# Performance work log

Measured on AMD Instinct MI355X. Metric: run time of the kernel, lower is better.

The kernel has to match this reference:

```python
import jax, jax.numpy as jnp
import numpy as np

E = 768; H = 64; W = 64; K = 3; PAD = 1
CH = [30, 100, 150, 220, 268]


def _conv3x3(x, w, b):
    out = jax.lax.conv_general_dilated(x, w, (1, 1), ((PAD, PAD), (PAD, PAD)),
                                       dimension_numbers=('NCHW', 'OIHW', 'NCHW'))
    return out + b[None, :, None, None]


def _deform_conv(x, offset, mask, w, b):
    # modulated deform_conv2d, group=1, stride=1, dil=1, pad=1 (torchvision semantics)
    N, C, Hh, Ww = x.shape
    KK = K * K
    off = offset.reshape(N, KK, 2, Hh, Ww)  # [...,0]=dy, [...,1]=dx per kernel tap
    ky = jnp.repeat(jnp.arange(K), K).astype(x.dtype)
    kx = jnp.tile(jnp.arange(K), K).astype(x.dtype)
    hg = jnp.arange(Hh, dtype=x.dtype)[None, None, :, None]
    wg = jnp.arange(Ww, dtype=x.dtype)[None, None, None, :]
    py = hg - PAD + ky[None, :, None, None] + off[:, :, 0]  # [N,9,H,W]
    px = wg - PAD + kx[None, :, None, None] + off[:, :, 1]
    y0 = jnp.floor(py); x0 = jnp.floor(px)
    xf = x.reshape(N, C, Hh * Ww)

    def gather(yi, xi):
        valid = ((yi >= 0) & (yi <= Hh - 1) & (xi >= 0) & (xi <= Ww - 1)).astype(x.dtype)
        yc = jnp.clip(yi, 0, Hh - 1).astype(jnp.int32)
        xc = jnp.clip(xi, 0, Ww - 1).astype(jnp.int32)
        idx = (yc * Ww + xc).reshape(N, 1, KK * Hh * Ww)
        g = jnp.take_along_axis(xf, idx, axis=2).reshape(N, C, KK, Hh, Ww)
        return g * valid[:, None]

    wy1 = py - y0; wx1 = px - x0; wy0 = 1.0 - wy1; wx0 = 1.0 - wx1
    samp = (gather(y0, x0) * (wy0 * wx0)[:, None]
            + gather(y0, x0 + 1) * (wy0 * wx1)[:, None]
            + gather(y0 + 1, x0) * (wy1 * wx0)[:, None]
            + gather(y0 + 1, x0 + 1) * (wy1 * wx1)[:, None])
    samp = samp * mask[:, None]  # modulation
    out = jnp.einsum('nckhw,ock->nohw', samp, w.reshape(w.shape[0], C, KK))
    return out + b[None, :, None, None]


def _block(x, conv_w, conv_b, off_w, off_b, msk_w, msk_b, bn_g, bn_b):
    # DefConv2d.forward: conv -> offset/mask linears -> deform conv -> BN(train stats) -> relu
    N, C, Hh, Ww = x.shape
    om = _conv3x3(x, conv_w, conv_b)
    om_hwc = om.transpose(0, 2, 3, 1)
    offset = (om_hwc @ off_w.T + off_b).transpose(0, 3, 1, 2)  # [N,18,H,W]
    mask = jax.nn.softmax(om_hwc @ msk_w.T + msk_b, axis=-1)   # [N,H,W,9]
    mask = mask.reshape(N, K * K, Hh, Ww)  # raw reshape, exactly as torch .reshape (no permute)
    out = _deform_conv(x, offset, mask, conv_w, conv_b)
    mu = out.mean(axis=(0, 2, 3), keepdims=True)
    var = out.var(axis=(0, 2, 3), keepdims=True)
    out = (out - mu) / jnp.sqrt(var + 1e-5) * bn_g[None, :, None, None] + bn_b[None, :, None, None]
    return jax.nn.relu(out)


def _cam(x, chq_w, chv_w, chz_w, ln_g, ln_b, spq_w, spv_w):
    xin = x
    N, C, Hh, Ww = x.shape  # N must be 1 (matches torch reshapes)
    # channel attention
    wv = jnp.einsum('nchw,oc->nohw', x, chv_w).reshape(C // 2, Hh * Ww)
    wq = jax.nn.softmax(jnp.einsum('nchw,oc->nohw', x, chq_w).reshape(Hh * Ww))
    wz = chz_w @ (wv @ wq)  # [C]
    wz = (wz - wz.mean()) / jnp.sqrt(wz.var() + 1e-5) * ln_g + ln_b
    x = jax.nn.sigmoid(wz)[None, :, None, None] * x
    # spatial attention
    wq = jax.nn.softmax(jnp.einsum('nchw,oc->nohw', x, spq_w).max(axis=(2, 3)).reshape(C // 2))
    wv = jnp.einsum('nchw,oc->nohw', x, spv_w).reshape(C // 2, Hh * Ww)
    wz = jax.nn.sigmoid(wq @ wv).reshape(1, 1, Hh, Ww)
    return wz * x + xin


def _forward(x1, x2, x3, x4, x5, conv_w, conv_b, off_w, off_b, msk_w, msk_b, bn_g, bn_b,
             chq_w, chv_w, chz_w, ln_g, ln_b, spq_w, spv_w,
             w1, w2, w3a, w3b, w4a, w4b, w5a, w5b, norm_g, norm_b):
    xper = [t.transpose(0, 3, 1, 2) for t in (x1, x2, x3, x4, x5)]
    blk = lambda t: _block(t, conv_w, conv_b, off_w, off_b, msk_w, msk_b, bn_g, bn_b)
    c1 = lambda t, w: jnp.einsum('nchw,oc->nohw', t, w)
    o1 = c1(blk(xper[0]), w1)
    o2 = c1(blk(xper[1]), w2)
    o3 = c1(blk(xper[2]), w3a) + c1(xper[2], w3b)
    o4 = c1(blk(xper[3]), w4a) + c1(xper[3], w4b)
    o5 = c1(blk(xper[4]), w5a) + c1(xper[4], w5b)
    out = jnp.concatenate((o1, o2, o3, o4, o5), axis=1)  # sum(CH)=768 channels
    out = _cam(out, chq_w, chv_w, chz_w, ln_g, ln_b, spq_w, spv_w)
    out = (out + xper[4]).transpose(0, 2, 3, 1)
    mu = out.mean(-1, keepdims=True)
    var = out.var(-1, keepdims=True)
    return (out - mu) / jnp.sqrt(var + 1e-5) * norm_g + norm_b


def setup_inputs() -> dict:
    key = jax.random.key(0)
    ks = iter(jax.random.split(key, 40))
    rnd = lambda shape, s=0.05: jax.random.normal(next(ks), shape, dtype=jnp.float32) * s
    d = {}
    for i in range(5):
        d[f'x{i+1}'] = jax.random.normal(next(ks), (1, H, W, E), dtype=jnp.float32)
    d['conv_w'] = rnd((E, E, 3, 3), 0.02)
    d['conv_b'] = jnp.zeros((E,), jnp.float32)
    d['off_w'] = rnd((2 * 9, E), 0.01); d['off_b'] = jnp.zeros((18,), jnp.float32)
    d['msk_w'] = rnd((9, E), 0.01); d['msk_b'] = jnp.zeros((9,), jnp.float32)
    d['bn_g'] = jnp.ones((E,), jnp.float32); d['bn_b'] = jnp.zeros((E,), jnp.float32)
    C = sum(CH)  # 768
    d['chq_w'] = rnd((1, C)); d['chv_w'] = rnd((C // 2, C)); d['chz_w'] = rnd((C, C // 2))
    d['ln_g'] = jnp.ones((C,), jnp.float32); d['ln_b'] = jnp.zeros((C,), jnp.float32)
    d['spq_w'] = rnd((C // 2, C)); d['spv_w'] = rnd((C // 2, C))
    d['w1'] = rnd((CH[0], E)); d['w2'] = rnd((CH[1], E))
    d['w3a'] = rnd((CH[2], E)); d['w3b'] = rnd((CH[2], E))
    d['w4a'] = rnd((CH[3], E)); d['w4b'] = rnd((CH[3], E))
    d['w5a'] = rnd((CH[4], E)); d['w5b'] = rnd((CH[4], E))
    d['norm_g'] = jnp.ones((E,), jnp.float32); d['norm_b'] = jnp.zeros((E,), jnp.float32)
    return d


def reference(x1, x2, x3, x4, x5, conv_w, conv_b, off_w, off_b, msk_w, msk_b, bn_g, bn_b,
              chq_w, chv_w, chz_w, ln_g, ln_b, spq_w, spv_w,
              w1, w2, w3a, w3b, w4a, w4b, w5a, w5b, norm_g, norm_b):
    return _forward(x1, x2, x3, x4, x5, conv_w, conv_b, off_w, off_b, msk_w, msk_b, bn_g, bn_b,
                    chq_w, chv_w, chz_w, ln_g, ln_b, spq_w, spv_w,
                    w1, w2, w3a, w3b, w4a, w4b, w5a, w5b, norm_g, norm_b)
```

## Files before the change

kernel.cpp:

```cpp
#include <hip/hip_runtime.h>
#include <cstdint>
#include <cstddef>

#define HW 4096
#define CDIM 768
#define PPIX 4356

typedef unsigned short u16;
typedef __attribute__((ext_vector_type(8))) short short8;
typedef __attribute__((ext_vector_type(4))) float f32x4;

__device__ __forceinline__ float bf2f(u16 u) { return __uint_as_float(((unsigned)u) << 16); }
__device__ __forceinline__ u16 f2bf(float f) {
    unsigned u = __float_as_uint(f);
    unsigned r = (u + 0x7fffu + ((u >> 16) & 1u)) >> 16;
    return (u16)r;
}
__device__ __forceinline__ float lof(unsigned u) { return __uint_as_float(u << 16); }
__device__ __forceinline__ float hif(unsigned u) { return __uint_as_float(u & 0xffff0000u); }
__device__ __forceinline__ int swz(int r) { return ((r >> 1) ^ (r >> 3)) & 3; }

__device__ __forceinline__ void gl16(const u16* g, u16* l) {
    __builtin_amdgcn_global_load_lds(
        (const __attribute__((address_space(1))) unsigned int*)g,
        (__attribute__((address_space(3))) unsigned int*)l, 16, 0, 0);
}

enum GMode { G_CONV = 0, G_PROJ = 2, G_SPAT = 3 };

struct ProjP {
    const u16* b1[5];
    const u16* b2[5];
    int ch[5];
    int choff[5];
};

template <int MODE>
__launch_bounds__(256, 4)
__global__ void k_gemm128(const u16* __restrict__ xpad, const u16* __restrict__ blkA,
                          const u16* __restrict__ Wt, const float* __restrict__ bias,
                          u16* __restrict__ outb, float* __restrict__ outf, ProjP pp) {
    const int z = blockIdx.z;
    const int m0 = blockIdx.x * 128;
    const int n0 = blockIdx.y * 128;

    int Nrows, ntap, choff = 0, ldo = CDIM;
    const u16 *Az = nullptr, *Ac = nullptr, *B1 = nullptr, *B2 = nullptr;
    if constexpr (MODE == G_CONV) {
        Az = xpad + (size_t)z * PPIX * CDIM; B1 = Wt; Nrows = 768; ntap = 9;
    } else if constexpr (MODE == G_PROJ) {
        Ac = blkA + (size_t)z * HW * CDIM;
        Az = xpad + (size_t)z * PPIX * CDIM;
        B1 = pp.b1[z]; B2 = pp.b2[z];
        Nrows = pp.ch[z]; choff = pp.choff[z];
        ntap = B2 ? 2 : 1;
        if (n0 >= Nrows) return;
    } else {
        Ac = blkA; B1 = Wt; Nrows = 384; ntap = 1; ldo = 384;
    }

    __shared__ __align__(16) u16 As[128 * 32];
    __shared__ __align__(16) u16 Bs[128 * 32];

    const int t = threadIdx.x;
    const int lane = t & 63;
    const int wid = t >> 6;
    const int wrow = (wid >> 1) * 64, wcol = (wid & 1) * 64;
    const int lm = lane & 15;
    const int quad = lane >> 4;

    const int rS = t >> 2;
    const int cs0 = (t & 3) ^ swz(rS);
    const int cs1 = (t & 3) ^ swz(64 + rS);

    const u16 *a0 = nullptr, *a1 = nullptr, *a0x = nullptr, *a1x = nullptr;
    if constexpr (MODE == G_CONV) {
        int p0 = m0 + rS, p1 = m0 + 64 + rS;
        a0 = Az + (size_t)(((p0 >> 6)) * 66 + (p0 & 63)) * CDIM + cs0 * 8;
        a1 = Az + (size_t)(((p1 >> 6)) * 66 + (p1 & 63)) * CDIM + cs1 * 8;
    } else if constexpr (MODE == G_PROJ) {
        int p0 = m0 + rS, p1 = m0 + 64 + rS;
        a0 = Ac + (size_t)p0 * CDIM + cs0 * 8;
        a1 = Ac + (size_t)p1 * CDIM + cs1 * 8;
        a0x = Az + (size_t)(((p0 >> 6) + 1) * 66 + (p0 & 63) + 1) * CDIM + cs0 * 8;
        a1x = Az + (size_t)(((p1 >> 6) + 1) * 66 + (p1 & 63) + 1) * CDIM + cs1 * 8;
    } else {
        a0 = Ac + (size_t)(m0 + rS) * CDIM + cs0 * 8;
        a1 = Ac + (size_t)(m0 + 64 + rS) * CDIM + cs1 * 8;
    }
    const u16* b0 = B1 + (size_t)(n0 + rS) * CDIM + cs0 * 8;
    const u16* b1p = B1 + (size_t)(n0 + 64 + rS) * CDIM + cs1 * 8;
    const u16 *c0 = nullptr, *c1 = nullptr;
    if constexpr (MODE == G_PROJ) {
        if (B2) {
            c0 = B2 + (size_t)(n0 + rS) * CDIM + cs0 * 8;
            c1 = B2 + (size_t)(n0 + 64 + rS) * CDIM + cs1 * 8;
        }
    }

    u16* dA0 = &As[(0 * 4 + wid) * 512];
    u16* dA1 = &As[(1 * 4 + wid) * 512];
    u16* dB0 = &Bs[(0 * 4 + wid) * 512];
    u16* dB1 = &Bs[(1 * 4 + wid) * 512];

    f32x4 acc[4][4];
#pragma unroll
    for (int i = 0; i < 4; i++)
#pragma unroll
        for (int j = 0; j < 4; j++) acc[i][j] = (f32x4){0.f, 0.f, 0.f, 0.f};

    const int totS = ntap * 24;
    int tap = 0;
    int tA = 0, tB = 0, kO = 0;

    for (int s = 0; s < totS; ++s) {
        __syncthreads();
        if constexpr (MODE == G_CONV) {
            gl16(a0 + tA + kO, dA0);
            gl16(a1 + tA + kO, dA1);
            gl16(b0 + tB + kO, dB0);
            gl16(b1p + tB + kO, dB1);
        } else if constexpr (MODE == G_PROJ) {
            if (tap == 0) {
                gl16(a0 + kO, dA0);
                gl16(a1 + kO, dA1);
                gl16(b0 + kO, dB0);
                gl16(b1p + kO, dB1);
            } else {
                gl16(a0x + kO, dA0);
                gl16(a1x + kO, dA1);
                gl16(c0 + kO, dB0);
                gl16(c1 + kO, dB1);
            }
        } else {
            gl16(a0 + kO, dA0);
            gl16(a1 + kO, dA1);
            gl16(b0 + kO, dB0);
            gl16(b1p + kO, dB1);
        }
        __syncthreads();
        short8 af[4], bf[4];
#pragma unroll
        for (int i = 0; i < 4; i++) {
            int rr = wrow + i * 16 + lm;
            af[i] = *(const short8*)&As[rr * 32 + ((quad ^ swz(rr)) * 8)];
        }
#pragma unroll
        for (int j = 0; j < 4; j++) {
            int rr = wcol + j * 16 + lm;
            bf[j] = *(const short8*)&Bs[rr * 32 + ((quad ^ swz(rr)) * 8)];
        }
#pragma unroll
        for (int i = 0; i < 4; i++)
#pragma unroll
            for (int j = 0; j < 4; j++)
                acc[i][j] = __builtin_amdgcn_mfma_f32_16x16x32_bf16(af[i], bf[j], acc[i][j], 0, 0, 0);
        tap++;
        if constexpr (MODE == G_CONV) {
            tA += (tap == 3 || tap == 6) ? 64 * CDIM : CDIM;
            tB += CDIM * CDIM;
            if (tap == 9) { tap = 0; tA = 0; tB = 0; kO += 32; }
        } else {
            if (tap == ntap) { tap = 0; kO += 32; }
        }
    }

    if constexpr (MODE == G_CONV) {
        u16* outz = outb + (size_t)z * HW * CDIM;
#pragma unroll
        for (int j = 0; j < 4; j++) {
            int gc = n0 + wcol + j * 16 + lm;
            float bv = bias[gc];
#pragma unroll
            for (int i = 0; i < 4; i++)
#pragma unroll
                for (int r = 0; r < 4; r++) {
                    int gr = m0 + wrow + i * 16 + quad * 4 + r;
                    outz[(size_t)gr * CDIM + gc] = f2bf(acc[i][j][r] + bv);
                }
        }
    } else {
#pragma unroll
        for (int j = 0; j < 4; j++) {
            int gc = n0 + wcol + j * 16 + lm;
            if (gc < Nrows) {
#pragma unroll
                for (int i = 0; i < 4; i++)
#pragma unroll
                    for (int r = 0; r < 4; r++) {
                        int gr = m0 + wrow + i * 16 + quad * 4 + r;
                        outf[(size_t)gr * ldo + choff + gc] = acc[i][j][r];
                    }
            }
        }
    }
}

__device__ __forceinline__ void xcd_decode(int bid, int& m0, int& n0, int& z) {
    int work = (bid & 7) * 60 + (bid >> 3);
    z = work / 96;
    int rem = work - z * 96;
    n0 = (rem >> 5) * 256;
    m0 = (rem & 31) * 128;
}

__global__ void k_fold(const u16* __restrict__ Wt, const float* __restrict__ off_w,
                       const float* __restrict__ msk_w, u16* __restrict__ OMW) {
    const int cb = blockIdx.x, tp = blockIdx.y, qg = blockIdx.z;
    const int q0 = qg * 9;
    __shared__ float ow[256 * 9];
    const int c = cb * 256 + threadIdx.x;
    const u16* wcol = Wt + (size_t)tp * 768 * 768 + c;
    float acc[9];
#pragma unroll
    for (int qi = 0; qi < 9; qi++) acc[qi] = 0.f;
    for (int ob = 0; ob < 768; ob += 256) {
        __syncthreads();
#pragma unroll
        for (int qi = 0; qi < 9; qi++) {
            int q = q0 + qi;
            const float* src = (q < 18) ? (off_w + (size_t)q * 768)
                                        : (msk_w + (size_t)(q - 18) * 768);
            ow[threadIdx.x * 9 + qi] = src[ob + threadIdx.x];
        }
        __syncthreads();
#pragma unroll 4
        for (int oo = 0; oo < 256; oo++) {
            float w = bf2f(wcol[(size_t)(ob + oo) * 768]);
#pragma unroll
            for (int qi = 0; qi < 9; qi++) acc[qi] = fmaf(w, ow[oo * 9 + qi], acc[qi]);
        }
    }
#pragma unroll
    for (int qi = 0; qi < 9; qi++)
        OMW[((size_t)tp * 32 + q0 + qi) * 768 + c] = f2bf(acc[qi]);
    if (qg == 2) {
        for (int q = 27; q < 32; q++) OMW[((size_t)tp * 32 + q) * 768 + c] = 0;
    }
}

__global__ void k_bias27(const float* __restrict__ off_w, const float* __restrict__ msk_w,
                         const float* __restrict__ conv_b, const float* __restrict__ off_b,
                         const float* __restrict__ msk_b, float* __restrict__ bb) {
    int wid = threadIdx.x >> 6, lane = threadIdx.x & 63;
    int q = blockIdx.x * 4 + wid;
    if (q >= 27) return;
    const float* r = (q < 18) ? (off_w + (size_t)q * 768) : (msk_w + (size_t)(q - 18) * 768);
    float s = 0.f;
#pragma unroll
    for (int j = 0; j < 12; j++) s += r[lane + 64 * j] * conv_b[lane + 64 * j];
#pragma unroll
    for (int o = 32; o > 0; o >>= 1) s += __shfl_xor(s, o, 64);
    if (lane == 0) bb[q] = s + ((q < 18) ? off_b[q] : msk_b[q - 18]);
}

__launch_bounds__(512, 4)
__global__ void k_convOM(const u16* __restrict__ xpad, const u16* __restrict__ OMW,
                         float* __restrict__ pOM) {
    const int z = blockIdx.z;
    const int part = blockIdx.y;
    const int m0 = blockIdx.x * 128;
    const u16* Az = xpad + (size_t)z * PPIX * CDIM + (size_t)part * 66 * CDIM;

    __shared__ __align__(16) u16 As[2][128 * 32];
    __shared__ __align__(16) u16 Bs[2][32 * 32];

    const int t = threadIdx.x;
    const int lane = t & 63;
    const int wid = t >> 6;
    const int lm = lane & 15;
    const int quad = lane >> 4;

    const int rA = t >> 2;
    const int cA = (t & 3) ^ swz(rA);
    const int p0 = m0 + rA;
    const u16* aB = Az + (size_t)((p0 >> 6) * 66 + (p0 & 63)) * CDIM + cA * 8;

    const int rB = t >> 2;
    const int cB = (t & 3) ^ swz(rB);
    const u16* bB = OMW + (size_t)(part * 3) * 32 * 768 + (size_t)rB * 768 + cB * 8;

    f32x4 acc[2];
    acc[0] = (f32x4){0.f, 0.f, 0.f, 0.f};
    acc[1] = (f32x4){0.f, 0.f, 0.f, 0.f};

    gl16(aB, &As[0][wid * 512]);
    if (t < 128) gl16(bB, &Bs[0][wid * 512]);

    int tloc = 0, tA = 0, tB = 0, kO = 0;
    for (int s = 0; s < 72; ++s) {
        const int cur = s & 1, nxt = cur ^ 1;
        __syncthreads();
        const bool hasN = (s + 1 < 72);
        if (hasN) {
            tloc++;
            tA += CDIM;
            tB += 32 * 768;
            if (tloc == 3) { tloc = 0; tA = 0; tB = 0; kO += 32; }
            gl16(aB + tA + kO, &As[nxt][wid * 512]);
            if (t < 128) gl16(bB + tB + kO, &Bs[nxt][wid * 512]);
        }
        int ar = wid * 16 + lm;
        short8 af = *(const short8*)&As[cur][ar * 32 + ((quad ^ swz(ar)) * 8)];
#pragma unroll
        for (int j = 0; j < 2; j++) {
            int rr = j * 16 + lm;
            short8 bf = *(const short8*)&Bs[cur][rr * 32 + ((quad ^ swz(rr)) * 8)];
            acc[j] = __builtin_amdgcn_mfma_f32_16x16x32_bf16(af, bf, acc[j], 0, 0, 0);
        }
    }

    float* outp = pOM + (((size_t)z * 3 + part) * HW) * 32;
#pragma unroll
    for (int j = 0; j < 2; j++) {
        int gc = j * 16 + lm;
#pragma unroll
        for (int r = 0; r < 4; r++) {
            int gr = m0 + wid * 16 + quad * 4 + r;
            outp[(size_t)gr * 32 + gc] = acc[j][r];
        }
    }
}

__global__ void k_omsum(const float* __restrict__ pOM, const float* __restrict__ bb,
                        float* __restrict__ offs, float* __restrict__ mlog) {
    int id = blockIdx.x * 256 + threadIdx.x;
    int q = id & 31;
    int p = (id >> 5) & 4095;
    int z = id >> 17;
    if (q >= 27) return;
    const float* base = pOM + (((size_t)z * 3) * HW + p) * 32 + q;
    float v = base[0] + base[(size_t)HW * 32] + base[(size_t)2 * HW * 32] + bb[q];
    if (q < 18) offs[((size_t)z * HW + p) * 18 + q] = v;
    else mlog[(size_t)z * 36864 + (size_t)p * 9 + (q - 18)] = v;
}

__launch_bounds__(512, 4)
__global__ void k_gdef(const u16* __restrict__ xpad, const u16* __restrict__ Wt,
                       const int4* __restrict__ idx4, const float4* __restrict__ w4,
                       const float* __restrict__ bias, u16* __restrict__ outb) {
    int m0, n0, z;
    xcd_decode(blockIdx.x, m0, n0, z);
    const u16* Az = xpad + (size_t)z * PPIX * CDIM;
    const int4* idxz = idx4 + (size_t)z * 9 * 4096;
    const float4* w4z = w4 + (size_t)z * 9 * 4096;

    __shared__ __align__(16) u16 As[2][128 * 32];
    __shared__ __align__(16) u16 Bs[2][256 * 32];

    const int t = threadIdx.x;
    const int lane = t & 63;
    const int wid = t >> 6;
    const int wrow = (wid >> 2) * 64, wcol = (wid & 3) * 64;
    const int lm = lane & 15;
    const int quad = lane >> 4;

    const int rA = t >> 2;
    const int cA = (t & 3) ^ swz(rA);
    const int rB0 = t >> 2;
    const int cB0 = (t & 3) ^ swz(rB0);
    const int rB1 = 128 + (t >> 2);
    const int cB1 = (t & 3) ^ swz(rB1);

    f32x4 acc[4][4];
#pragma unroll
    for (int i = 0; i < 4; i++)
#pragma unroll
        for (int j = 0; j < 4; j++) acc[i][j] = (f32x4){0.f, 0.f, 0.f, 0.f};

    const u16* bP0;
    const u16* bP1;
    int dOff[4];
    float4 wv;

    auto setupSub = [&](int sn) {
        const u16* Bb = Wt + (size_t)sn * CDIM * CDIM;
        bP0 = Bb + (size_t)(n0 + rB0) * CDIM + cB0 * 8;
        bP1 = Bb + (size_t)(n0 + rB1) * CDIM + cB1 * 8;
        int4 iv = idxz[sn * 4096 + m0 + rA];
        wv = w4z[sn * 4096 + m0 + rA];
        dOff[0] = (iv.x + cA * 8) * 2;
        dOff[1] = (iv.y + cA * 8) * 2;
        dOff[2] = (iv.z + cA * 8) * 2;
        dOff[3] = (iv.w + cA * 8) * 2;
    };

    auto blend4 = [&](const uint4* L) -> uint4 {
        auto bl = [&](unsigned a, unsigned b, unsigned c2, unsigned d) -> unsigned {
            float lo = fmaf(wv.x, lof(a), fmaf(wv.y, lof(b), fmaf(wv.z, lof(c2), wv.w * lof(d))));
            float hi = fmaf(wv.x, hif(a), fmaf(wv.y, hif(b), fmaf(wv.z, hif(c2), wv.w * hif(d))));
            return __builtin_amdgcn_perm(__float_as_uint(hi), __float_as_uint(lo), 0x07060302u);
        };
        uint4 o;
        o.x = bl(L[0].x, L[1].x, L[2].x, L[3].x);
        o.y = bl(L[0].y, L[1].y, L[2].y, L[3].y);
        o.z = bl(L[0].z, L[1].z, L[2].z, L[3].z);
        o.w = bl(L[0].w, L[1].w, L[2].w, L[3].w);
        return o;
    };

    setupSub(0);
    int stagedSub = 0;

    {
        uint4 L[4];
#pragma unroll
        for (int k = 0; k < 4; k++)
            L[k] = *(const uint4*)((const char*)Az + dOff[k]);
        gl16(bP0, &Bs[0][wid * 512]);
        gl16(bP1, &Bs[0][4096 + wid * 512]);
        uint4 o = blend4(L);
        *(uint4*)&As[0][t * 8] = o;
    }

    for (int s = 0; s < 216; ++s) {
        const int cur = s & 1;
        const int nxt = cur ^ 1;
        __syncthreads();
        const bool hasN = (s + 1 < 216);
        uint4 L[4];
        if (hasN) {
            int kn = (s + 1) - stagedSub * 24;
            if (kn == 24) { setupSub(++stagedSub); kn = 0; }
            const int cb = kn * 64;
#pragma unroll
            for (int k = 0; k < 4; k++)
                L[k] = *(const uint4*)((const char*)Az + dOff[k] + cb);
            gl16(bP0 + kn * 32, &Bs[nxt][wid * 512]);
            gl16(bP1 + kn * 32, &Bs[nxt][4096 + wid * 512]);
        }
        short8 af[4];
#pragma unroll
        for (int i = 0; i < 4; i++) {
            int rr = wrow + i * 16 + lm;
            af[i] = *(const short8*)&As[cur][rr * 32 + ((quad ^ swz(rr)) * 8)];
        }
#pragma unroll
        for (int j = 0; j < 4; j++) {
            int rr = wcol + j * 16 + lm;
            short8 bf = *(const short8*)&Bs[cur][rr * 32 + ((quad ^ swz(rr)) * 8)];
#pragma unroll
            for (int i = 0; i < 4; i++)
                acc[i][j] = __builtin_amdgcn_mfma_f32_16x16x32_bf16(af[i], bf, acc[i][j], 0, 0, 0);
        }
        if (hasN) {
            uint4 o = blend4(L);
            *(uint4*)&As[nxt][t * 8] = o;
        }
    }

    u16* outz = outb + (size_t)z * HW * CDIM;
#pragma unroll
    for (int j = 0; j < 4; j++) {
        int gc = n0 + wcol + j * 16 + lm;
        float bv = bias[gc];
#pragma unroll
        for (int i = 0; i < 4; i++)
#pragma unroll
            for (int r = 0; r < 4; r++) {
                int gr = m0 + wrow + i * 16 + quad * 4 + r;
                outz[(size_t)gr * CDIM + gc] = f2bf(acc[i][j][r] + bv);
            }
    }
}

struct Ptr5 { const float* p[5]; };

__global__ void k_prep_xpad(Ptr5 xs, u16* __restrict__ xpad) {
    int z = blockIdx.y;
    int pidx = blockIdx.x;
    int ph = pidx / 66, pw = pidx - ph * 66;
    int e0 = threadIdx.x * 4;
    u16* d = xpad + ((size_t)z * PPIX + pidx) * CDIM + e0;
    if (ph == 0 || ph == 65 || pw == 0 || pw == 65) {
        *(uint2*)d = make_uint2(0, 0);
        return;
    }
    const float* s = xs.p[z] + ((size_t)((ph - 1) * 64 + (pw - 1))) * CDIM + e0;
    float4 v = *(const float4*)s;
    u16 o[4] = {f2bf(v.x), f2bf(v.y), f2bf(v.z), f2bf(v.w)};
    *(uint2*)d = *(uint2*)o;
}

__global__ void k_prep_wt(const float* __restrict__ cw, u16* __restrict__ Wt) {
    int o = blockIdx.x;
    for (int c = threadIdx.x; c < 768; c += 256) {
        const float* s = cw + ((size_t)o * 768 + c) * 9;
#pragma unroll
        for (int k = 0; k < 9; k++)
            Wt[(size_t)k * 768 * 768 + (size_t)o * 768 + c] = f2bf(s[k]);
    }
}

struct WbP { const float* src[9]; u16* dst[9]; int n[9]; };

__global__ void k_prep_wb(WbP wp) {
    int m = blockIdx.y;
    int i = (blockIdx.x * 256 + threadIdx.x) * 4;
    if (i >= wp.n[m]) return;
    float4 v = *(const float4*)(wp.src[m] + i);
    u16* d = wp.dst[m] + i;
    d[0] = f2bf(v.x); d[1] = f2bf(v.y); d[2] = f2bf(v.z); d[3] = f2bf(v.w);
}

__device__ __forceinline__ int cidx(int y, int x) {
    int yc = min(max(y, 0), 63), xc = min(max(x, 0), 63);
    return ((yc + 1) * 66 + (xc + 1)) * CDIM;
}
__device__ __forceinline__ float cval(int y, int x) {
    return (y >= 0 && y < 64 && x >= 0 && x < 64) ? 1.f : 0.f;
}

__global__ void k_offmask2(const float* __restrict__ offs, const float* __restrict__ mlog,
                           int4* __restrict__ idx4o, float4* __restrict__ w4o) {
    int id = blockIdx.x * 256 + threadIdx.x;
    int z = id / 36864, r = id % 36864, k = r >> 12, p = r & 4095;
    const float* ofz = offs + ((size_t)z * HW + p) * 18;
    float dy = ofz[2 * k], dx = ofz[2 * k + 1];
    int flat = k * 4096 + p;
    int P = flat / 9, jj = flat - P * 9;
    const float* ml = mlog + (size_t)z * 36864 + (size_t)P * 9;
    float l[9], mx = -1e30f;
#pragma unroll
    for (int i2 = 0; i2 < 9; i2++) { l[i2] = ml[i2]; mx = fmaxf(mx, l[i2]); }
    float sum = 0.f;
#pragma unroll
    for (int i2 = 0; i2 < 9; i2++) sum += expf(l[i2] - mx);
    float mk = expf(l[jj] - mx) / sum;
    int h = p >> 6, w = p & 63;
    float py = (float)(h - 1 + k / 3) + dy;
    float px = (float)(w - 1 + k % 3) + dx;
    float y0f = floorf(py), x0f = floorf(px);
    int y0 = (int)y0f, x0 = (int)x0f;
    float wy1 = py - y0f, wx1 = px - x0f, wy0 = 1.f - wy1, wx0 = 1.f - wx1;
    idx4o[id] = make_int4(cidx(y0, x0), cidx(y0, x0 + 1), cidx(y0 + 1, x0), cidx(y0 + 1, x0 + 1));
    w4o[id] = make_float4(wy0 * wx0 * cval(y0, x0) * mk, wy0 * wx1 * cval(y0, x0 + 1) * mk,
                          wy1 * wx0 * cval(y0 + 1, x0) * mk, wy1 * wx1 * cval(y0 + 1, x0 + 1) * mk);
}

__global__ void k_bnstats2(const u16* __restrict__ dout, float* __restrict__ pb1,
                           float* __restrict__ pb2) {
    const int z = blockIdx.z, seg = blockIdx.y;
    const int cx = threadIdx.x & 7, py = threadIdx.x >> 3;
    const int c0 = blockIdx.x * 64 + cx * 8;
    const u16* base = dout + (size_t)z * HW * CDIM + (size_t)(seg * 1024) * CDIM + c0;
    float s1[8] = {0.f, 0.f, 0.f, 0.f, 0.f, 0.f, 0.f, 0.f};
    float s2[8] = {0.f, 0.f, 0.f, 0.f, 0.f, 0.f, 0.f, 0.f};
    for (int p = py; p < 1024; p += 32) {
        uint4 v = *(const uint4*)(base + (size_t)p * CDIM);
        const u16* u = (const u16*)&v;
#pragma unroll
        for (int e = 0; e < 8; e++) {
            float f = bf2f(u[e]);
            s1[e] += f; s2[e] += f * f;
        }
    }
    __shared__ float l1[32][64], l2[32][64];
#pragma unroll
    for (int e = 0; e < 8; e++) {
        l1[py][cx * 8 + e] = s1[e];
        l2[py][cx * 8 + e] = s2[e];
    }
    __syncthreads();
    if (threadIdx.x < 64) {
        float a = 0.f, b = 0.f;
        for (int y = 0; y < 32; y++) { a += l1[y][threadIdx.x]; b += l2[y][threadIdx.x]; }
        int ch = blockIdx.x * 64 + threadIdx.x;
        pb1[(z * 4 + seg) * 768 + ch] = a;
        pb2[(z * 4 + seg) * 768 + ch] = b;
    }
}

__global__ void k_bnfinal(const float* __restrict__ pb1, const float* __restrict__ pb2,
                          float* __restrict__ mu, float* __restrict__ rs) {
    int i = blockIdx.x * 256 + threadIdx.x;
    if (i >= 3840) return;
    int z = i / 768, ch = i % 768;
    float a = 0.f, b = 0.f;
#pragma unroll
    for (int s = 0; s < 4; s++) {
        a += pb1[(z * 4 + s) * 768 + ch];
        b += pb2[(z * 4 + s) * 768 + ch];
    }
    float m = a / 4096.f;
    float var = b / 4096.f - m * m;
    mu[i] = m;
    rs[i] = rsqrtf(var + 1e-5f);
}

__global__ void k_bnapply(const u16* __restrict__ dout, const float* __restrict__ mu,
                          const float* __restrict__ rs, const float* __restrict__ g,
                          const float* __restrict__ b, u16* __restrict__ blk) {
    size_t i = ((size_t)blockIdx.x * 256 + threadIdx.x) * 8;
    int c = (int)(i % CDIM);
    int z = (int)(i / ((size_t)HW * CDIM));
    const float* muz = mu + z * 768;
    const float* rsz = rs + z * 768;
    uint4 in = *(const uint4*)(dout + i);
    const u16* u = (const u16*)&in;
    u16 o[8];
#pragma unroll
    for (int e = 0; e < 8; e++) {
        int ce = c + e;
        float v = (bf2f(u[e]) - muz[ce]) * rsz[ce] * g[ce] + b[ce];
        o[e] = f2bf(fmaxf(v, 0.f));
    }
    *(uint4*)(blk + i) = *(uint4*)o;
}

__global__ void k_q(const float* __restrict__ X, const float* __restrict__ chq,
                    float* __restrict__ q) {
    int wid = threadIdx.x >> 6, lane = threadIdx.x & 63;
    int p = blockIdx.x * 4 + wid;
    const float* xr = X + (size_t)p * CDIM;
    float s = 0.f;
#pragma unroll
    for (int j = 0; j < 12; j++) s += xr[lane + 64 * j] * chq[lane + 64 * j];
#pragma unroll
    for (int o = 32; o > 0; o >>= 1) s += __shfl_xor(s, o, 64);
    if (lane == 0) q[p] = s;
}

__global__ void k_soft4096(const float* __restrict__ q, float* __restrict__ sqn,
                           float* __restrict__ xq) {
    __shared__ float red[4];
    int tid = threadIdx.x, lane = tid & 63, wid = tid >> 6;
    float m = -1e30f;
    for (int i = tid; i < 4096; i += 256) m = fmaxf(m, q[i]);
    for (int o = 32; o > 0; o >>= 1) m = fmaxf(m, __shfl_xor(m, o, 64));
    if (lane == 0) red[wid] = m;
    __syncthreads();
    float bm = fmaxf(fmaxf(red[0], red[1]), fmaxf(red[2], red[3]));
    __syncthreads();
    float s = 0.f;
    for (int i = tid; i < 4096; i += 256) {
        float e = expf(q[i] - bm);
        sqn[i] = e; s += e;
    }
    for (int o = 32; o > 0; o >>= 1) s += __shfl_xor(s, o, 64);
    if (lane == 0) red[wid] = s;
    __syncthreads();
    float inv = 1.f / (red[0] + red[1] + red[2] + red[3]);
    for (int i = tid; i < 4096; i += 256) sqn[i] *= inv;
    for (int c = tid; c < 768; c += 256) xq[c] = 0.f;
}

__global__ void k_xq(const float* __restrict__ X, const float* __restrict__ sqn,
                     float* __restrict__ xq) {
    int p0 = blockIdx.x * 128;
    for (int c = threadIdx.x; c < 768; c += 256) {
        float a = 0.f;
        for (int p = p0; p < p0 + 128; p++) a += sqn[p] * X[(size_t)p * CDIM + c];
        atomicAdd(&xq[c], a);
    }
}

__global__ void k_gemv384(const float* __restrict__ chv, const float* __restrict__ xq,
                          float* __restrict__ wvq) {
    int wid = threadIdx.x >> 6, lane = threadIdx.x & 63;
    int o = blockIdx.x * 4 + wid;
    const float* r = chv + (size_t)o * 768;
    float s = 0.f;
#pragma unroll
    for (int j = 0; j < 12; j++) s += r[lane + 64 * j] * xq[lane + 64 * j];
#pragma unroll
    for (int off = 32; off > 0; off >>= 1) s += __shfl_xor(s, off, 64);
    if (lane == 0) wvq[o] = s;
}

__global__ void k_gemv768(const float* __restrict__ chz, const float* __restrict__ wvq,
                          float* __restrict__ wzv) {
    int wid = threadIdx.x >> 6, lane = threadIdx.x & 63;
    int c = blockIdx.x * 4 + wid;
    const float* r = chz + (size_t)c * 384;
    float s = 0.f;
#pragma unroll
    for (int j = 0; j < 6; j++) s += r[lane + 64 * j] * wvq[lane + 64 * j];
#pragma unroll
    for (int off = 32; off > 0; off >>= 1) s += __shfl_xor(s, off, 64);
    if (lane == 0) wzv[c] = s;
}

__global__ void k_lngate(const float* __restrict__ wzv, const float* __restrict__ lng,
                         const float* __restrict__ lnb, float* __restrict__ sgate) {
    __shared__ float red[8];
    int tid = threadIdx.x, lane = tid & 63, wid = tid >> 6;
    float a = wzv[tid], b = wzv[tid + 256], c = wzv[tid + 512];
    float s1 = a + b + c, s2 = a * a + b * b + c * c;
    for (int o = 32; o > 0; o >>= 1) { s1 += __shfl_xor(s1, o, 64); s2 += __shfl_xor(s2, o, 64); }
    if (lane == 0) { red[wid] = s1; red[4 + wid] = s2; }
    __syncthreads();
    s1 = red[0] + red[1] + red[2] + red[3];
    s2 = red[4] + red[5] + red[6] + red[7];
    float mean = s1 / 768.f, var = s2 / 768.f - mean * mean, rstd = rsqrtf(var + 1e-5f);
    for (int cc = tid; cc < 768; cc += 256) {
        float tv = (wzv[cc] - mean) * rstd * lng[cc] + lnb[cc];
        sgate[cc] = 1.f / (1.f + expf(-tv));
    }
}

__global__ void k_xatt(const float* __restrict__ X, const float* __restrict__ sgate,
                       u16* __restrict__ xatt) {
    size_t i = ((size_t)blockIdx.x * 256 + threadIdx.x) * 4;
    int c = (int)(i % CDIM);
    float4 v = *(const float4*)(X + i);
    u16 o[4] = {f2bf(v.x * sgate[c]), f2bf(v.y * sgate[c + 1]),
                f2bf(v.z * sgate[c + 2]), f2bf(v.w * sgate[c + 3])};
    *(uint2*)(xatt + i) = *(uint2*)o;
}

__global__ void k_colmax24(const float* __restrict__ P2, float* __restrict__ m2) {
    __shared__ float red[16][17];
    int col = blockIdx.x * 16 + threadIdx.x;
    float m = -1e30f;
    for (int p = threadIdx.y; p < 4096; p += 16) m = fmaxf(m, P2[(size_t)p * 384 + col]);
    red[threadIdx.y][threadIdx.x] = m;
    __syncthreads();
    if (threadIdx.y == 0) {
        for (int y = 1; y < 16; y++) m = fmaxf(m, red[y][threadIdx.x]);
        m2[col] = m;
    }
}

__global__ void k_sm384(const float* __restrict__ m2, float* __restrict__ sq2) {
    __shared__ float red[6];
    int tid = threadIdx.x, lane = tid & 63, wid = tid >> 6;
    float v = m2[tid];
    float m = v;
    for (int o = 32; o > 0; o >>= 1) m = fmaxf(m, __shfl_xor(m, o, 64));
    if (lane == 0) red[wid] = m;
    __syncthreads();
    m = red[0];
    for (int w = 1; w < 6; w++) m = fmaxf(m, red[w]);
    __syncthreads();
    float e = expf(v - m);
    float s = e;
    for (int o = 32; o > 0; o >>= 1) s += __shfl_xor(s, o, 64);
    if (lane == 0) red[wid] = s;
    __syncthreads();
    float tot = 0.f;
    for (int w = 0; w < 6; w++) tot += red[w];
    sq2[tid] = e / tot;
}

__global__ void k_sv(const float* __restrict__ sq2, const float* __restrict__ spv,
                     float* __restrict__ sv) {
    __shared__ float part[4][64];
    int c = blockIdx.x * 64 + (threadIdx.x & 63);
    int seg = threadIdx.x >> 6;
    float a = 0.f;
    for (int o = seg * 96; o < seg * 96 + 96; o++) a += sq2[o] * spv[(size_t)o * 768 + c];
    part[seg][threadIdx.x & 63] = a;
    __syncthreads();
    if (seg == 0) sv[c] = part[0][threadIdx.x] + part[1][threadIdx.x] +
                          part[2][threadIdx.x] + part[3][threadIdx.x];
}

__global__ void k_final(const float* __restrict__ X, const float* __restrict__ x5,
                        const float* __restrict__ sgate, const float* __restrict__ sv,
                        const float* __restrict__ ng, const float* __restrict__ nb,
                        float* __restrict__ out) {
    int wid = threadIdx.x >> 6, lane = threadIdx.x & 63;
    int p = blockIdx.x * 4 + wid;
    const float* xr = X + (size_t)p * CDIM;
    const float* x5r = x5 + (size_t)p * CDIM;
    float xa[12];
    float d = 0.f;
#pragma unroll
    for (int j = 0; j < 12; j++) {
        int c = lane + 64 * j;
        float a = xr[c] * sgate[c];
        xa[j] = a;
        d += sv[c] * a;
    }
#pragma unroll
    for (int o = 32; o > 0; o >>= 1) d += __shfl_xor(d, o, 64);
    float wz2 = 1.f / (1.f + expf(-d));
    float s1 = 0.f, s2 = 0.f;
#pragma unroll
    for (int j = 0; j < 12; j++) {
        int c = lane + 64 * j;
        float y = wz2 * xa[j] + xr[c] + x5r[c];
        xa[j] = y;
        s1 += y; s2 += y * y;
    }
#pragma unroll
    for (int o = 32; o > 0; o >>= 1) { s1 += __shfl_xor(s1, o, 64); s2 += __shfl_xor(s2, o, 64); }
    float mean = s1 / 768.f, var = s2 / 768.f - mean * mean, rstd = rsqrtf(var + 1e-5f);
#pragma unroll
    for (int j = 0; j < 12; j++) {
        int c = lane + 64 * j;
        out[(size_t)p * CDIM + c] = (xa[j] - mean) * rstd * ng[c] + nb[c];
    }
}

extern "C" void kernel_launch(void* const* d_in, const int* in_sizes, int n_in,
                              void* d_out, int out_size, void* d_ws, size_t ws_size,
                              hipStream_t stream) {
    const float* xin[5];
    for (int i = 0; i < 5; i++) xin[i] = (const float*)d_in[i];
    const float* conv_w = (const float*)d_in[5];
    const float* conv_b = (const float*)d_in[6];
    const float* off_w = (const float*)d_in[7];
    const float* off_b = (const float*)d_in[8];
    const float* msk_w = (const float*)d_in[9];
    const float* msk_b = (const float*)d_in[10];
    const float* bn_g = (const float*)d_in[11];
    const float* bn_b = (const float*)d_in[12];
    const float* chq_w = (const float*)d_in[13];
    const float* chv_w = (const float*)d_in[14];
    const float* chz_w = (const float*)d_in[15];
    const float* ln_g = (const float*)d_in[16];
    const float* ln_b = (const float*)d_in[17];
    const float* spq_w = (const float*)d_in[18];
    const float* spv_w = (const float*)d_in[19];
    const float* wsrc[8];
    for (int i = 0; i < 8; i++) wsrc[i] = (const float*)d_in[20 + i];
    const float* norm_g = (const float*)d_in[28];
    const float* norm_b = (const float*)d_in[29];
    float* out = (float*)d_out;

    char* wsb = (char*)d_ws;
    size_t off = 0;
    auto take = [&](size_t n) -> char* {
        char* p = wsb + off;
        off = (off + n + 255) & ~(size_t)255;
        return p;
    };
    u16* xpad = (u16*)take(5ll * PPIX * CDIM * 2);
    u16* Wt = (u16*)take(9ll * CDIM * CDIM * 2);
    u16* omblk = (u16*)take(5ll * HW * CDIM * 2);
    float* offs = (float*)take(5ll * HW * 18 * 4);
    float* mlog = (float*)take(5ll * 36864 * 4);
    int4* idx4 = (int4*)take(5ll * 9 * 4096 * 16);
    float4* w4 = (float4*)take(5ll * 9 * 4096 * 16);
    u16* dout = (u16*)take(5ll * HW * CDIM * 2);
    u16* wb = (u16*)take(1790ll * 768 * 2);
    u16* OMW = (u16*)take(9ll * 32 * 768 * 2);
    float* bb = (float*)take(32 * 4);
    float* pOM = (float*)take(5ll * 3 * HW * 32 * 4);
    float* Xcat = (float*)take((size_t)HW * CDIM * 4);
    float* mu = (float*)take(5 * 768 * 4);
    float* rs = (float*)take(5 * 768 * 4);
    float* pb1 = (float*)take(5 * 4 * 768 * 4);
    float* pb2 = (float*)take(5 * 4 * 768 * 4);
    float* qv = (float*)take(4096 * 4);
    float* sqn = (float*)take(4096 * 4);
    float* xq = (float*)take(768 * 4);
    float* wvq = (float*)take(384 * 4);
    float* wzv = (float*)take(768 * 4);
    float* sgate = (float*)take(768 * 4);
    float* m2 = (float*)take(384 * 4);
    float* sq2 = (float*)take(384 * 4);
    float* sv = (float*)take(768 * 4);
    u16* xatt = dout;
    float* P2 = (float*)((char*)dout + 8388608);
    u16* blk = omblk;
    (void)ws_size; (void)in_sizes; (void)n_in; (void)out_size;

    int rows[9] = {30, 100, 150, 150, 220, 220, 268, 268, 384};
    int roff[9]; int acc = 0;
    for (int i = 0; i < 9; i++) { roff[i] = acc; acc += rows[i]; }
    u16* spqb = wb + (size_t)roff[8] * 768;

    WbP wp;
    for (int i = 0; i < 8; i++) { wp.src[i] = wsrc[i]; wp.dst[i] = wb + (size_t)roff[i] * 768; wp.n[i] = rows[i] * 768; }
    wp.src[8] = spq_w; wp.dst[8] = spqb; wp.n[8] = rows[8] * 768;

    ProjP pp;
    pp.b1[0] = wb + (size_t)roff[0] * 768; pp.b2[0] = nullptr;
    pp.b1[1] = wb + (size_t)roff[1] * 768; pp.b2[1] = nullptr;
    pp.b1[2] = wb + (size_t)roff[2] * 768; pp.b2[2] = wb + (size_t)roff[3] * 768;
    pp.b1[3] = wb + (size_t)roff[4] * 768; pp.b2[3] = wb + (size_t)roff[5] * 768;
    pp.b1[4] = wb + (size_t)roff[6] * 768; pp.b2[4] = wb + (size_t)roff[7] * 768;
    int chs[5] = {30, 100, 150, 220, 268};
    int cof[5] = {0, 30, 130, 280, 500};
    for (int i = 0; i < 5; i++) { pp.ch[i] = chs[i]; pp.choff[i] = cof[i]; }
    ProjP pdum = {};

    Ptr5 xs;
    for (int i = 0; i < 5; i++) xs.p[i] = xin[i];

    k_prep_xpad<<<dim3(PPIX, 5), 192, 0, stream>>>(xs, xpad);
    k_prep_wt<<<dim3(768), 256, 0, stream>>>(conv_w, Wt);
    k_prep_wb<<<dim3(288, 9), 256, 0, stream>>>(wp);
    k_fold<<<dim3(3, 9, 3), 256, 0, stream>>>(Wt, off_w, msk_w, OMW);
    k_bias27<<<dim3(7), 256, 0, stream>>>(off_w, msk_w, conv_b, off_b, msk_b, bb);

    k_convOM<<<dim3(32, 3, 5), 512, 0, stream>>>(xpad, OMW, pOM);
    k_omsum<<<dim3(2560), 256, 0, stream>>>(pOM, bb, offs, mlog);
    k_offmask2<<<dim3(720), 256, 0, stream>>>(offs, mlog, idx4, w4);
    k_gdef<<<dim3(480), 512, 0, stream>>>(xpad, Wt, idx4, w4, conv_b, dout);
    k_bnstats2<<<dim3(12, 4, 5), 256, 0, stream>>>(dout, pb1, pb2);
    k_bnfinal<<<dim3(15), 256, 0, stream>>>(pb1, pb2, mu, rs);
    k_bnapply<<<dim3(7680), 256, 0, stream>>>(dout, mu, rs, bn_g, bn_b, blk);
    k_gemm128<G_PROJ><<<dim3(32, 3, 5), 256, 0, stream>>>(xpad, blk, nullptr, nullptr,
                                                          nullptr, Xcat, pp);

    k_q<<<dim3(1024), 256, 0, stream>>>(Xcat, chq_w, qv);
    k_soft4096<<<dim3(1), 256, 0, stream>>>(qv, sqn, xq);
    k_xq<<<dim3(32), 256, 0, stream>>>(Xcat, sqn, xq);
    k_gemv384<<<dim3(96), 256, 0, stream>>>(chv_w, xq, wvq);
    k_gemv768<<<dim3(192), 256, 0, stream>>>(chz_w, wvq, wzv);
    k_lngate<<<dim3(1), 256, 0, stream>>>(wzv, ln_g, ln_b, sgate);
    k_xatt<<<dim3(3072), 256, 0, stream>>>(Xcat, sgate, xatt);
    k_gemm128<G_SPAT><<<dim3(32, 3, 1), 256, 0, stream>>>(xpad, xatt, spqb, nullptr,
                                                          nullptr, P2, pdum);
    k_colmax24<<<dim3(24), dim3(16, 16), 0, stream>>>(P2, m2);
    k_sm384<<<dim3(1), 384, 0, stream>>>(m2, sq2);
    k_sv<<<dim3(12), 256, 0, stream>>>(sq2, spv_w, sv);

    k_final<<<dim3(1024), 256, 0, stream>>>(Xcat, xin[4], sgate, sv, norm_g, norm_b, out);
}
```

Before: 821.6 us.

## Fuse BN stats into deform GEMM epilogue and merge small reduction kernels

BatchNorm sum and sum-of-squares are now accumulated in the deformable-conv GEMM epilogue, using LDS atomics followed by global atomics. This removes the separate pass that re-read the bf16 output. The three-way partial-sum kernel for the offset and mask maps is folded into the offset/mask kernel, the 4096-wide softmax is folded into the xq reduction, and the 384-wide softmax is folded into the sv GEMV. The goal is fewer launches and less global traffic. The cost is extra atomic contention, redundant softmax work in each block, and BN stats taken from fp32 values rather than rounded bf16 ones.

New measurement: 800.6 us. -2.6%, faster.

```diff
diff --git a/kernel.cpp b/kernel.cpp
--- a/kernel.cpp
+++ b/kernel.cpp
@@ -322,23 +322,11 @@
     }
 }
 
-__global__ void k_omsum(const float* __restrict__ pOM, const float* __restrict__ bb,
-                        float* __restrict__ offs, float* __restrict__ mlog) {
-    int id = blockIdx.x * 256 + threadIdx.x;
-    int q = id & 31;
-    int p = (id >> 5) & 4095;
-    int z = id >> 17;
-    if (q >= 27) return;
-    const float* base = pOM + (((size_t)z * 3) * HW + p) * 32 + q;
-    float v = base[0] + base[(size_t)HW * 32] + base[(size_t)2 * HW * 32] + bb[q];
-    if (q < 18) offs[((size_t)z * HW + p) * 18 + q] = v;
-    else mlog[(size_t)z * 36864 + (size_t)p * 9 + (q - 18)] = v;
-}
-
 __launch_bounds__(512, 4)
 __global__ void k_gdef(const u16* __restrict__ xpad, const u16* __restrict__ Wt,
                        const int4* __restrict__ idx4, const float4* __restrict__ w4,
-                       const float* __restrict__ bias, u16* __restrict__ outb) {
+                       const float* __restrict__ bias, u16* __restrict__ outb,
+                       float* __restrict__ pb1, float* __restrict__ pb2) {
     int m0, n0, z;
     xcd_decode(blockIdx.x, m0, n0, z);
     const u16* Az = xpad + (size_t)z * PPIX * CDIM;
@@ -347,6 +335,7 @@
 
     __shared__ __align__(16) u16 As[2][128 * 32];
     __shared__ __align__(16) u16 Bs[2][256 * 32];
+    __shared__ float r1[256], r2[256];
 
     const int t = threadIdx.x;
     const int lane = t & 63;
@@ -449,18 +438,31 @@
         }
     }
 
+    if (t < 256) { r1[t] = 0.f; r2[t] = 0.f; }
+    __syncthreads();
     u16* outz = outb + (size_t)z * HW * CDIM;
 #pragma unroll
     for (int j = 0; j < 4; j++) {
         int gc = n0 + wcol + j * 16 + lm;
         float bv = bias[gc];
+        float s1 = 0.f, s2 = 0.f;
 #pragma unroll
         for (int i = 0; i < 4; i++)
 #pragma unroll
             for (int r = 0; r < 4; r++) {
                 int gr = m0 + wrow + i * 16 + quad * 4 + r;
-                outz[(size_t)gr * CDIM + gc] = f2bf(acc[i][j][r] + bv);
+                float v = acc[i][j][r] + bv;
+                outz[(size_t)gr * CDIM + gc] = f2bf(v);
+                s1 += v;
+                s2 += v * v;
             }
+        atomicAdd(&r1[wcol + j * 16 + lm], s1);
+        atomicAdd(&r2[wcol + j * 16 + lm], s2);
+    }
+    __syncthreads();
+    if (t < 256) {
+        atomicAdd(&pb1[z * 768 + n0 + t], r1[t]);
+        atomicAdd(&pb2[z * 768 + n0 + t], r2[t]);
     }
 }
 
@@ -511,18 +513,27 @@
     return (y >= 0 && y < 64 && x >= 0 && x < 64) ? 1.f : 0.f;
 }
 
-__global__ void k_offmask2(const float* __restrict__ offs, const float* __restrict__ mlog,
+__global__ void k_offmask2(const float* __restrict__ pOM, const float* __restrict__ bb,
+                           float* __restrict__ pb1, float* __restrict__ pb2,
                            int4* __restrict__ idx4o, float4* __restrict__ w4o) {
+    if (blockIdx.x == 0) {
+        for (int i = threadIdx.x; i < 3840; i += 256) { pb1[i] = 0.f; pb2[i] = 0.f; }
+    }
     int id = blockIdx.x * 256 + threadIdx.x;
     int z = id / 36864, r = id % 36864, k = r >> 12, p = r & 4095;
-    const float* ofz = offs + ((size_t)z * HW + p) * 18;
-    float dy = ofz[2 * k], dx = ofz[2 * k + 1];
+    const size_t ps = (size_t)HW * 32;
+    const float* P0 = pOM + (size_t)z * 3 * ps + (size_t)p * 32;
+    float dy = P0[2 * k] + P0[ps + 2 * k] + P0[2 * ps + 2 * k] + bb[2 * k];
+    float dx = P0[2 * k + 1] + P0[ps + 2 * k + 1] + P0[2 * ps + 2 * k + 1] + bb[2 * k + 1];
     int flat = k * 4096 + p;
     int P = flat / 9, jj = flat - P * 9;
-    const float* ml = mlog + (size_t)z * 36864 + (size_t)P * 9;
+    const float* Q0 = pOM + (size_t)z * 3 * ps + (size_t)P * 32 + 18;
     float l[9], mx = -1e30f;
 #pragma unroll
-    for (int i2 = 0; i2 < 9; i2++) { l[i2] = ml[i2]; mx = fmaxf(mx, l[i2]); }
+    for (int i2 = 0; i2 < 9; i2++) {
+        l[i2] = Q0[i2] + Q0[ps + i2] + Q0[2 * ps + i2] + bb[18 + i2];
+        mx = fmaxf(mx, l[i2]);
+    }
     float sum = 0.f;
 #pragma unroll
     for (int i2 = 0; i2 < 9; i2++) sum += expf(l[i2] - mx);
@@ -538,50 +549,12 @@
                           wy1 * wx0 * cval(y0 + 1, x0) * mk, wy1 * wx1 * cval(y0 + 1, x0 + 1) * mk);
 }
 
-__global__ void k_bnstats2(const u16* __restrict__ dout, float* __restrict__ pb1,
-                           float* __restrict__ pb2) {
-    const int z = blockIdx.z, seg = blockIdx.y;
-    const int cx = threadIdx.x & 7, py = threadIdx.x >> 3;
-    const int c0 = blockIdx.x * 64 + cx * 8;
-    const u16* base = dout + (size_t)z * HW * CDIM + (size_t)(seg * 1024) * CDIM + c0;
-    float s1[8] = {0.f, 0.f, 0.f, 0.f, 0.f, 0.f, 0.f, 0.f};
-    float s2[8] = {0.f, 0.f, 0.f, 0.f, 0.f, 0.f, 0.f, 0.f};
-    for (int p = py; p < 1024; p += 32) {
-        uint4 v = *(const uint4*)(base + (size_t)p * CDIM);
-        const u16* u = (const u16*)&v;
-#pragma unroll
-        for (int e = 0; e < 8; e++) {
-            float f = bf2f(u[e]);
-            s1[e] += f; s2[e] += f * f;
-        }
-    }
-    __shared__ float l1[32][64], l2[32][64];
-#pragma unroll
-    for (int e = 0; e < 8; e++) {
-        l1[py][cx * 8 + e] = s1[e];
-        l2[py][cx * 8 + e] = s2[e];
-    }
-    __syncthreads();
-    if (threadIdx.x < 64) {
-        float a = 0.f, b = 0.f;
-        for (int y = 0; y < 32; y++) { a += l1[y][threadIdx.x]; b += l2[y][threadIdx.x]; }
-        int ch = blockIdx.x * 64 + threadIdx.x;
-        pb1[(z * 4 + seg) * 768 + ch] = a;
-        pb2[(z * 4 + seg) * 768 + ch] = b;
-    }
-}
-
 __global__ void k_bnfinal(const float* __restrict__ pb1, const float* __restrict__ pb2,
                           float* __restrict__ mu, float* __restrict__ rs) {
     int i = blockIdx.x * 256 + threadIdx.x;
     if (i >= 3840) return;
-    int z = i / 768, ch = i % 768;
-    float a = 0.f, b = 0.f;
-#pragma unroll
-    for (int s = 0; s < 4; s++) {
-        a += pb1[(z * 4 + s) * 768 + ch];
-        b += pb2[(z * 4 + s) * 768 + ch];
-    }
+    float a = pb1[i];
+    float b = pb2[i];
     float m = a / 4096.f;
     float var = b / 4096.f - m * m;
     mu[i] = m;
@@ -609,7 +582,10 @@
 }
 
 __global__ void k_q(const float* __restrict__ X, const float* __restrict__ chq,
-                    float* __restrict__ q) {
+                    float* __restrict__ q, float* __restrict__ xq) {
+    if (blockIdx.x == 0) {
+        for (int c = threadIdx.x; c < 768; c += 256) xq[c] = 0.f;
+    }
     int wid = threadIdx.x >> 6, lane = threadIdx.x & 63;
     int p = blockIdx.x * 4 + wid;
     const float* xr = X + (size_t)p * CDIM;
@@ -621,36 +597,29 @@
     if (lane == 0) q[p] = s;
 }
 
-__global__ void k_soft4096(const float* __restrict__ q, float* __restrict__ sqn,
-                           float* __restrict__ xq) {
-    __shared__ float red[4];
+__global__ void k_xq(const float* __restrict__ X, const float* __restrict__ qv,
+                     float* __restrict__ xq) {
+    __shared__ float red[8];
+    __shared__ float sq[128];
     int tid = threadIdx.x, lane = tid & 63, wid = tid >> 6;
     float m = -1e30f;
-    for (int i = tid; i < 4096; i += 256) m = fmaxf(m, q[i]);
+    for (int i = tid; i < 4096; i += 256) m = fmaxf(m, qv[i]);
     for (int o = 32; o > 0; o >>= 1) m = fmaxf(m, __shfl_xor(m, o, 64));
     if (lane == 0) red[wid] = m;
     __syncthreads();
     float bm = fmaxf(fmaxf(red[0], red[1]), fmaxf(red[2], red[3]));
-    __syncthreads();
     float s = 0.f;
-    for (int i = tid; i < 4096; i += 256) {
-        float e = expf(q[i] - bm);
-        sqn[i] = e; s += e;
-    }
+    for (int i = tid; i < 4096; i += 256) s += expf(qv[i] - bm);
     for (int o = 32; o > 0; o >>= 1) s += __shfl_xor(s, o, 64);
-    if (lane == 0) red[wid] = s;
-    __syncthreads();
-    float inv = 1.f / (red[0] + red[1] + red[2] + red[3]);
-    for (int i = tid; i < 4096; i += 256) sqn[i] *= inv;
-    for (int c = tid; c < 768; c += 256) xq[c] = 0.f;
-}
-
-__global__ void k_xq(const float* __restrict__ X, const float* __restrict__ sqn,
-                     float* __restrict__ xq) {
+    if (lane == 0) red[4 + wid] = s;
+    __syncthreads();
+    float inv = 1.f / (red[4] + red[5] + red[6] + red[7]);
     int p0 = blockIdx.x * 128;
-    for (int c = threadIdx.x; c < 768; c += 256) {
+    if (tid < 128) sq[tid] = expf(qv[p0 + tid] - bm) * inv;
+    __syncthreads();
+    for (int c = tid; c < 768; c += 256) {
         float a = 0.f;
-        for (int p = p0; p < p0 + 128; p++) a += sqn[p] * X[(size_t)p * CDIM + c];
+        for (int p = 0; p < 128; p++) a += sq[p] * X[(size_t)(p0 + p) * CDIM + c];
         atomicAdd(&xq[c], a);
     }
 }
@@ -722,38 +691,36 @@
     }
 }
 
-__global__ void k_sm384(const float* __restrict__ m2, float* __restrict__ sq2) {
-    __shared__ float red[6];
+__global__ void k_sv(const float* __restrict__ m2, const float* __restrict__ spv,
+                     float* __restrict__ sv) {
+    __shared__ float part[4][64];
+    __shared__ float red[8];
+    __shared__ float sq2l[384];
     int tid = threadIdx.x, lane = tid & 63, wid = tid >> 6;
-    float v = m2[tid];
-    float m = v;
+    float x1 = m2[tid];
+    float x2 = (tid < 128) ? m2[tid + 256] : -1e30f;
+    float m = fmaxf(x1, x2);
     for (int o = 32; o > 0; o >>= 1) m = fmaxf(m, __shfl_xor(m, o, 64));
     if (lane == 0) red[wid] = m;
     __syncthreads();
-    m = red[0];
-    for (int w = 1; w < 6; w++) m = fmaxf(m, red[w]);
-    __syncthreads();
-    float e = expf(v - m);
-    float s = e;
+    m = fmaxf(fmaxf(red[0], red[1]), fmaxf(red[2], red[3]));
+    float e1 = expf(x1 - m);
+    float e2 = (tid < 128) ? expf(x2 - m) : 0.f;
+    float s = e1 + e2;
     for (int o = 32; o > 0; o >>= 1) s += __shfl_xor(s, o, 64);
-    if (lane == 0) red[wid] = s;
-    __syncthreads();
-    float tot = 0.f;
-    for (int w = 0; w < 6; w++) tot += red[w];
-    sq2[tid] = e / tot;
-}
-
-__global__ void k_sv(const float* __restrict__ sq2, const float* __restrict__ spv,
-                     float* __restrict__ sv) {
-    __shared__ float part[4][64];
-    int c = blockIdx.x * 64 + (threadIdx.x & 63);
-    int seg = threadIdx.x >> 6;
+    if (lane == 0) red[4 + wid] = s;
+    __syncthreads();
+    float inv = 1.f / (red[4] + red[5] + red[6] + red[7]);
+    sq2l[tid] = e1 * inv;
+    if (tid < 128) sq2l[tid + 256] = e2 * inv;
+    __syncthreads();
+    int c = blockIdx.x * 64 + (tid & 63);
+    int seg = tid >> 6;
     float a = 0.f;
-    for (int o = seg * 96; o < seg * 96 + 96; o++) a += sq2[o] * spv[(size_t)o * 768 + c];
-    part[seg][threadIdx.x & 63] = a;
-    __syncthreads();
-    if (seg == 0) sv[c] = part[0][threadIdx.x] + part[1][threadIdx.x] +
-                          part[2][threadIdx.x] + part[3][threadIdx.x];
+    for (int o = seg * 96; o < seg * 96 + 96; o++) a += sq2l[o] * spv[(size_t)o * 768 + c];
+    part[seg][tid & 63] = a;
+    __syncthreads();
+    if (seg == 0) sv[c] = part[0][tid] + part[1][tid] + part[2][tid] + part[3][tid];
 }
 
 __global__ void k_final(const float* __restrict__ X, const float* __restrict__ x5,
@@ -830,8 +797,6 @@
     u16* xpad = (u16*)take(5ll * PPIX * CDIM * 2);
     u16* Wt = (u16*)take(9ll * CDIM * CDIM * 2);
     u16* omblk = (u16*)take(5ll * HW * CDIM * 2);
-    float* offs = (float*)take(5ll * HW * 18 * 4);
-    float* mlog = (float*)take(5ll * 36864 * 4);
     int4* idx4 = (int4*)take(5ll * 9 * 4096 * 16);
     float4* w4 = (float4*)take(5ll * 9 * 4096 * 16);
     u16* dout = (u16*)take(5ll * HW * CDIM * 2);
@@ -842,16 +807,14 @@
     float* Xcat = (float*)take((size_t)HW * CDIM * 4);
     float* mu = (float*)take(5 * 768 * 4);
     float* rs = (float*)take(5 * 768 * 4);
-    float* pb1 = (float*)take(5 * 4 * 768 * 4);
-    float* pb2 = (float*)take(5 * 4 * 768 * 4);
+    float* pb1 = (float*)take(5 * 768 * 4);
+    float* pb2 = (float*)take(5 * 768 * 4);
     float* qv = (float*)take(4096 * 4);
-    float* sqn = (float*)take(4096 * 4);
     float* xq = (float*)take(768 * 4);
     float* wvq = (float*)take(384 * 4);
     float* wzv = (float*)take(768 * 4);
     float* sgate = (float*)take(768 * 4);
     float* m2 = (float*)take(384 * 4);
-    float* sq2 = (float*)take(384 * 4);
     float* sv = (float*)take(768 * 4);
     u16* xatt = dout;
     float* P2 = (float*)((char*)dout + 8388608);
@@ -888,18 +851,15 @@
     k_bias27<<<dim3(7), 256, 0, stream>>>(off_w, msk_w, conv_b, off_b, msk_b, bb);
 
     k_convOM<<<dim3(32, 3, 5), 512, 0, stream>>>(xpad, OMW, pOM);
-    k_omsum<<<dim3(2560), 256, 0, stream>>>(pOM, bb, offs, mlog);
-    k_offmask2<<<dim3(720), 256, 0, stream>>>(offs, mlog, idx4, w4);
-    k_gdef<<<dim3(480), 512, 0, stream>>>(xpad, Wt, idx4, w4, conv_b, dout);
-    k_bnstats2<<<dim3(12, 4, 5), 256, 0, stream>>>(dout, pb1, pb2);
+    k_offmask2<<<dim3(720), 256, 0, stream>>>(pOM, bb, pb1, pb2, idx4, w4);
+    k_gdef<<<dim3(480), 512, 0, stream>>>(xpad, Wt, idx4, w4, conv_b, dout, pb1, pb2);
     k_bnfinal<<<dim3(15), 256, 0, stream>>>(pb1, pb2, mu, rs);
     k_bnapply<<<dim3(7680), 256, 0, stream>>>(dout, mu, rs, bn_g, bn_b, blk);
     k_gemm128<G_PROJ><<<dim3(32, 3, 5), 256, 0, stream>>>(xpad, blk, nullptr, nullptr,
                                                           nullptr, Xcat, pp);
 
-    k_q<<<dim3(1024), 256, 0, stream>>>(Xcat, chq_w, qv);
-    k_soft4096<<<dim3(1), 256, 0, stream>>>(qv, sqn, xq);
-    k_xq<<<dim3(32), 256, 0, stream>>>(Xcat, sqn, xq);
+    k_q<<<dim3(1024), 256, 0, stream>>>(Xcat, chq_w, qv, xq);
+    k_xq<<<dim3(32), 256, 0, stream>>>(Xcat, qv, xq);
     k_gemv384<<<dim3(96), 256, 0, stream>>>(chv_w, xq, wvq);
     k_gemv768<<<dim3(192), 256, 0, stream>>>(chz_w, wvq, wzv);
     k_lngate<<<dim3(1), 256, 0, stream>>>(wzv, ln_g, ln_b, sgate);
@@ -907,8 +867,7 @@
     k_gemm128<G_SPAT><<<dim3(32, 3, 1), 256, 0, stream>>>(xpad, xatt, spqb, nullptr,
                                                           nullptr, P2, pdum);
     k_colmax24<<<dim3(24), dim3(16, 16), 0, stream>>>(P2, m2);
-    k_sm384<<<dim3(1), 384, 0, stream>>>(m2, sq2);
-    k_sv<<<dim3(12), 256, 0, stream>>>(sq2, spv_w, sv);
+    k_sv<<<dim3(12), 256, 0, stream>>>(m2, spv_w, sv);
 
     k_final<<<dim3(1024), 256, 0, stream>>>(Xcat, xin[4], sgate, sv, norm_g, norm_b, out);
 }
```
